# Optimization experiments

Hardware: AMD Instinct MI355X
Metric: run time of the kernel (lower is better)

## Reference

```python
import jax, jax.numpy as jnp
import numpy as np

P = 16          # patch_size
C = 3           # in_chans
D = 768         # embed_dim
V = 10240       # position_embedding_size
B, H, W = 16, 512, 512
N = (H // P) * (W // P)  # 1024 patches per image


def setup_inputs() -> dict:
    key = jax.random.key(0)
    k1, k2, k3, k4, k5 = jax.random.split(key, 5)
    pixel_values = jax.random.uniform(k1, (B, C, H, W), dtype=jnp.float32)
    position_ids = jax.random.randint(k2, (B, N, 2), 0, 32)  # (x, y) patch coords < pW/pH
    padding_positions = jax.random.randint(k3, (B, N), 0, 2).astype(jnp.bool_)
    w_proj = jax.random.normal(k4, (D, C * P * P), dtype=jnp.float32) * 0.02  # Linear weight (out, in)
    pos_table = jax.random.normal(k5, (2, V, D), dtype=jnp.float32) * 0.02
    return {
        "pixel_values": pixel_values,
        "w_proj": w_proj,
        "pos_table": pos_table,
        "position_ids": position_ids,
        "padding_positions": padding_positions,
    }


def reference(pixel_values, w_proj, pos_table, position_ids, padding_positions):
    b, c, h, w = pixel_values.shape
    ph, pw = h // P, w // P
    # Extract patches in Gemma4 C-P-P flatten order: (B, N, C*P*P)
    x = pixel_values.reshape(b, c, ph, P, pw, P)
    x = jnp.transpose(x, (0, 2, 4, 1, 3, 5)).reshape(b, ph * pw, c * P * P)
    patches = 2.0 * (x - 0.5)
    hidden = jnp.einsum('bnf,df->bnd', patches, w_proj)
    # Position embeddings: one_hot(ids) @ table summed over the 2 axes
    # == direct gather-add: table[0][x_id] + table[1][y_id]
    ids = jnp.clip(position_ids, 0)
    pos = pos_table[0][ids[..., 0]] + pos_table[1][ids[..., 1]]  # (B, N, D)
    pos = jnp.where(padding_positions[..., None], 0.0, pos)
    return hidden + pos
```

## Files before the change

kernel.cpp:

```cpp
#include <hip/hip_runtime.h>
#include <stdint.h>


typedef __attribute__((ext_vector_type(8))) short bfrag_t;
typedef __attribute__((ext_vector_type(4))) float f4_t;
typedef __attribute__((ext_vector_type(4))) unsigned short u16x4;

#define V_POS 10240
#define RS 40
#define ABUF 5120

__device__ __forceinline__ unsigned short f2bf(float f) {
    unsigned int u = __float_as_uint(f);
    u += 0x7fffu + ((u >> 16) & 1u);
    return (unsigned short)(u >> 16);
}

__device__ __forceinline__ void lgkm_barrier() {
    __builtin_amdgcn_s_waitcnt(0xC07F);
    __builtin_amdgcn_s_barrier();
}

__global__ __launch_bounds__(256, 2) void fused_kernel(
    const float* __restrict__ px, const float* __restrict__ wp,
    const int* __restrict__ pos_ids, const unsigned int* __restrict__ pad_in,
    const float* __restrict__ pos_table, float* __restrict__ out)
{
    __shared__ unsigned short LDS[4 * ABUF];

    const int tid  = threadIdx.x;
    const int wave = tid >> 6;
    const int lane = tid & 63;

    const int id   = blockIdx.x;
    const int xcd  = id & 7;
    const int slot = id >> 3;
    const int bmg  = slot / 6;
    const int bm   = xcd * 16 + bmg;
    const int bn   = slot - bmg * 6;
    const int m0   = bm << 7;
    const int n0   = bn << 7;
    const int bimg = bm >> 3;
    const int ph0  = (bm & 7) << 2;

    const bool u8mode = __any(pad_in[lane] > 1u);

    int aw[4], bw[4], bgb[4];
#pragma unroll
    for (int j = 0; j < 4; ++j) {
        int f4A = j * 64 + lane;
        int kh  = f4A >> 7;
        int f4i = f4A & 127;
        int pw  = f4i >> 2;
        int e   = f4i & 3;
        aw[j] = (wave * 32 + pw) * RS + kh * 16 + e * 4;
        int offb = j * 1024 + lane * 16;
        int colL = offb >> 7;
        int win  = offb & 127;
        bgb[j] = colL * 3072 + win;
        bw[j]  = (wave * 32 + colL) * RS + (win >> 2);
    }
    const float* abase = px + (((size_t)bimg * 3) * 512 + (size_t)(ph0 + wave) * 16) * 512;
    const char*  bbase = (const char*)(wp + (size_t)(n0 + wave * 32) * 768);
    const int    aglo  = lane * 4;

    float4 FA[2][4], FB[2][4];

    auto load_tile = [&](int t) {
        int s = t & 1;
        const float* ab = abase + (t >> 3) * 262144 + ((t * 2) & 15) * 512;
#pragma unroll
        for (int j = 0; j < 4; ++j)
            FA[s][j] = *(const float4*)(ab + j * 256 + aglo);
        const char* bb = bbase + t * 128;
#pragma unroll
        for (int j = 0; j < 4; ++j)
            FB[s][j] = *(const float4*)(bb + bgb[j]);
    };
    auto store_tile = [&](int t) {
        int s = t & 1;
        unsigned short* A = LDS + s * ABUF;
        unsigned short* B = LDS + 2 * ABUF + s * ABUF;
#pragma unroll
        for (int j = 0; j < 4; ++j) {
            u16x4 v;
            v[0] = f2bf(2.f * FA[s][j].x - 1.f);
            v[1] = f2bf(2.f * FA[s][j].y - 1.f);
            v[2] = f2bf(2.f * FA[s][j].z - 1.f);
            v[3] = f2bf(2.f * FA[s][j].w - 1.f);
            *(u16x4*)(A + aw[j]) = v;
            u16x4 w;
            w[0] = f2bf(FB[s][j].x);
            w[1] = f2bf(FB[s][j].y);
            w[2] = f2bf(FB[s][j].z);
            w[3] = f2bf(FB[s][j].w);
            *(u16x4*)(B + bw[j]) = w;
        }
    };

    const int fr      = lane & 15;
    const int quad    = lane >> 4;
    const int row_off = (wave & 1) << 6;
    const int col_off = (wave >> 1) << 6;

    f4_t acc[4][4] = {};

    load_tile(0);
    load_tile(1);
    store_tile(0);
    lgkm_barrier();

#pragma unroll
    for (int kk = 0; kk < 24; ++kk) {
        if (kk < 22) load_tile(kk + 2);
        if (kk < 23) store_tile(kk + 1);
        const unsigned short* Ab = LDS + (kk & 1) * ABUF + (row_off + fr) * RS + quad * 8;
        const unsigned short* Bb = LDS + 2 * ABUF + (kk & 1) * ABUF + (col_off + fr) * RS + quad * 8;
        bfrag_t a[4], b[4];
#pragma unroll
        for (int i = 0; i < 4; ++i) a[i] = *(const bfrag_t*)(Ab + i * 16 * RS);
#pragma unroll
        for (int i = 0; i < 4; ++i) b[i] = *(const bfrag_t*)(Bb + i * 16 * RS);
#pragma unroll
        for (int mi = 0; mi < 4; ++mi)
#pragma unroll
            for (int ni = 0; ni < 4; ++ni)
                acc[mi][ni] = __builtin_amdgcn_mfma_f32_16x16x32_bf16(
                    a[mi], b[ni], acc[mi][ni], 0, 0, 0);
        if (kk < 23) lgkm_barrier();
    }

    const unsigned char* pad8 = (const unsigned char*)pad_in;
    const int colbase = n0 + col_off;
#pragma unroll
    for (int mi = 0; mi < 4; ++mi) {
#pragma unroll
        for (int reg = 0; reg < 4; ++reg) {
            int gm  = m0 + row_off + mi * 16 + (quad << 2) + reg;
            int xid = pos_ids[2 * gm];
            int yid = pos_ids[2 * gm + 1];
            xid = xid < 0 ? 0 : xid;
            yid = yid < 0 ? 0 : yid;
            bool p = u8mode ? (pad8[gm] != 0) : (pad_in[gm] != 0u);
            const float* t0 = pos_table + (size_t)xid * 768 + colbase;
            const float* t1 = pos_table + (size_t)(V_POS + yid) * 768 + colbase;
            float* orow = out + (size_t)gm * 768 + colbase;
#pragma unroll
            for (int ni = 0; ni < 4; ++ni) {
                int cc = ni * 16 + fr;
                float pos = p ? 0.f : (t0[cc] + t1[cc]);
                orow[cc] = acc[mi][ni][reg] + pos;
            }
        }
    }
}

extern "C" void kernel_launch(void* const* d_in, const int* in_sizes, int n_in,
                              void* d_out, int out_size, void* d_ws, size_t ws_size,
                              hipStream_t stream) {
    const float*        px  = (const float*)d_in[0];
    const float*        wp  = (const float*)d_in[1];
    const float*        pt  = (const float*)d_in[2];
    const int*          pid = (const int*)d_in[3];
    const unsigned int* pad = (const unsigned int*)d_in[4];

    fused_kernel<<<768, 256, 0, stream>>>(px, wp, pid, pad, pt, (float*)d_out);
}
```

Before: 177.3 us.

## Split into bf16 prep kernel and async-LDS triple-buffered GEMM

Moves the patch extraction, normalization and bf16 conversion of pixels and weights into a separate prep kernel that writes a bf16 patch matrix and weight matrix to the workspace. The GEMM kernel then streams the bf16 tiles directly into LDS with global_load_lds, using a triple-buffered, XOR-swizzled layout and fewer barriers. The goal is to take the conversion work and register staging out of the main loop and overlap the loads better. In exchange it adds an extra launch and a round trip of the bf16 intermediates through global memory.

```diff
diff --git a/kernel.cpp b/kernel.cpp
--- a/kernel.cpp
+++ b/kernel.cpp
@@ -4,11 +4,10 @@
 
 typedef __attribute__((ext_vector_type(8))) short bfrag_t;
 typedef __attribute__((ext_vector_type(4))) float f4_t;
+typedef __attribute__((ext_vector_type(8))) unsigned short u16x8;
 typedef __attribute__((ext_vector_type(4))) unsigned short u16x4;
 
 #define V_POS 10240
-#define RS 40
-#define ABUF 5120
 
 __device__ __forceinline__ unsigned short f2bf(float f) {
     unsigned int u = __float_as_uint(f);
@@ -16,17 +15,62 @@
     return (unsigned short)(u >> 16);
 }
 
-__device__ __forceinline__ void lgkm_barrier() {
-    __builtin_amdgcn_s_waitcnt(0xC07F);
-    __builtin_amdgcn_s_barrier();
+__device__ __forceinline__ void async_ld16(const void* g, void* l) {
+    __builtin_amdgcn_global_load_lds(
+        (const __attribute__((address_space(1))) void*)g,
+        (__attribute__((address_space(3))) void*)l, 16, 0, 0);
 }
 
-__global__ __launch_bounds__(256, 2) void fused_kernel(
+__global__ __launch_bounds__(256) void prep_kernel(
     const float* __restrict__ px, const float* __restrict__ wp,
+    unsigned short* __restrict__ A, unsigned short* __restrict__ Wb)
+{
+    __shared__ unsigned short T[32 * 776];
+    int bid = blockIdx.x, tid = threadIdx.x;
+    if (bid < 512) {
+        int b = bid >> 5, ph = bid & 31;
+        const float* pxb = px + ((size_t)b * 3 * 512 + (size_t)ph * 16) * 512;
+#pragma unroll 6
+        for (int it = 0; it < 24; ++it) {
+            int idx = it * 256 + tid;
+            int c = idx >> 11, rem = idx & 2047, hl = rem >> 7, w4 = rem & 127;
+            float4 v = *(const float4*)(pxb + (size_t)c * 262144 + hl * 512 + (w4 << 2));
+            int pw  = w4 >> 2;
+            int pxo = (w4 & 3) << 2;
+            int k   = c * 256 + hl * 16 + pxo;
+            u16x4 o;
+            o[0] = f2bf(2.f * v.x - 1.f);
+            o[1] = f2bf(2.f * v.y - 1.f);
+            o[2] = f2bf(2.f * v.z - 1.f);
+            o[3] = f2bf(2.f * v.w - 1.f);
+            *(u16x4*)&T[pw * 776 + k] = o;
+        }
+        __syncthreads();
+        int r = tid >> 3, p = tid & 7;
+        unsigned short* Arow = A + ((size_t)bid * 32 + r) * 768;
+        const unsigned short* Trow = T + r * 776;
+#pragma unroll 4
+        for (int j = 0; j < 12; ++j) {
+            int co = (p + 8 * j) << 3;
+            *(u16x8*)(Arow + co) = *(const u16x8*)(Trow + co);
+        }
+    } else {
+        long idx = (long)(bid - 512) * 256 + tid;
+        const float4* s = (const float4*)(wp + (idx << 3));
+        float4 v0 = s[0], v1 = s[1];
+        u16x8 o;
+        o[0] = f2bf(v0.x); o[1] = f2bf(v0.y); o[2] = f2bf(v0.z); o[3] = f2bf(v0.w);
+        o[4] = f2bf(v1.x); o[5] = f2bf(v1.y); o[6] = f2bf(v1.z); o[7] = f2bf(v1.w);
+        *(u16x8*)(Wb + (idx << 3)) = o;
+    }
+}
+
+__global__ __launch_bounds__(256, 3) void gemm_kernel(
+    const unsigned short* __restrict__ A, const unsigned short* __restrict__ Bt,
     const int* __restrict__ pos_ids, const unsigned int* __restrict__ pad_in,
     const float* __restrict__ pos_table, float* __restrict__ out)
 {
-    __shared__ unsigned short LDS[4 * ABUF];
+    __shared__ unsigned short LDS[3 * 8192];
 
     const int tid  = threadIdx.x;
     const int wave = tid >> 6;
@@ -40,94 +84,65 @@
     const int bn   = slot - bmg * 6;
     const int m0   = bm << 7;
     const int n0   = bn << 7;
-    const int bimg = bm >> 3;
-    const int ph0  = (bm & 7) << 2;
 
     const bool u8mode = __any(pad_in[lane] > 1u);
 
-    int aw[4], bw[4], bgb[4];
-#pragma unroll
-    for (int j = 0; j < 4; ++j) {
-        int f4A = j * 64 + lane;
-        int kh  = f4A >> 7;
-        int f4i = f4A & 127;
-        int pw  = f4i >> 2;
-        int e   = f4i & 3;
-        aw[j] = (wave * 32 + pw) * RS + kh * 16 + e * 4;
-        int offb = j * 1024 + lane * 16;
-        int colL = offb >> 7;
-        int win  = offb & 127;
-        bgb[j] = colL * 3072 + win;
-        bw[j]  = (wave * 32 + colL) * RS + (win >> 2);
-    }
-    const float* abase = px + (((size_t)bimg * 3) * 512 + (size_t)(ph0 + wave) * 16) * 512;
-    const char*  bbase = (const char*)(wp + (size_t)(n0 + wave * 32) * 768);
-    const int    aglo  = lane * 4;
-
-    float4 FA[2][4], FB[2][4];
-
-    auto load_tile = [&](int t) {
-        int s = t & 1;
-        const float* ab = abase + (t >> 3) * 262144 + ((t * 2) & 15) * 512;
-#pragma unroll
-        for (int j = 0; j < 4; ++j)
-            FA[s][j] = *(const float4*)(ab + j * 256 + aglo);
-        const char* bb = bbase + t * 128;
-#pragma unroll
-        for (int j = 0; j < 4; ++j)
-            FB[s][j] = *(const float4*)(bb + bgb[j]);
-    };
-    auto store_tile = [&](int t) {
-        int s = t & 1;
-        unsigned short* A = LDS + s * ABUF;
-        unsigned short* B = LDS + 2 * ABUF + s * ABUF;
-#pragma unroll
-        for (int j = 0; j < 4; ++j) {
-            u16x4 v;
-            v[0] = f2bf(2.f * FA[s][j].x - 1.f);
-            v[1] = f2bf(2.f * FA[s][j].y - 1.f);
-            v[2] = f2bf(2.f * FA[s][j].z - 1.f);
-            v[3] = f2bf(2.f * FA[s][j].w - 1.f);
-            *(u16x4*)(A + aw[j]) = v;
-            u16x4 w;
-            w[0] = f2bf(FB[s][j].x);
-            w[1] = f2bf(FB[s][j].y);
-            w[2] = f2bf(FB[s][j].z);
-            w[3] = f2bf(FB[s][j].w);
-            *(u16x4*)(B + bw[j]) = w;
-        }
-    };
+    const int rl = lane >> 2;
+    const int g  = (lane & 3) ^ (rl & 3);
+    const unsigned short* aga0 = A  + (size_t)(m0 + wave * 32 + rl) * 768 + g * 8;
+    const unsigned short* aga1 = aga0 + (size_t)16 * 768;
+    const unsigned short* bga0 = Bt + (size_t)(n0 + wave * 32 + rl) * 768 + g * 8;
+    const unsigned short* bga1 = bga0 + (size_t)16 * 768;
+    const int l0 = wave * 32 * 32;
+    const int l1 = l0 + 16 * 32;
 
     const int fr      = lane & 15;
     const int quad    = lane >> 4;
     const int row_off = (wave & 1) << 6;
     const int col_off = (wave >> 1) << 6;
+    const int afro = (row_off + fr) * 32 + ((quad ^ (fr & 3)) << 3);
+    const int bfro = (col_off + fr) * 32 + ((quad ^ (fr & 3)) << 3) + 4096;
 
     f4_t acc[4][4] = {};
 
-    load_tile(0);
-    load_tile(1);
-    store_tile(0);
-    lgkm_barrier();
+    auto issue = [&](int t, int b) {
+        unsigned short* Ab = (unsigned short*)LDS + b * 8192;
+        unsigned short* Bb = Ab + 4096;
+        const int ko = t * 32;
+        async_ld16(aga0 + ko, Ab + l0);
+        async_ld16(aga1 + ko, Ab + l1);
+        async_ld16(bga0 + ko, Bb + l0);
+        async_ld16(bga1 + ko, Bb + l1);
+    };
 
-#pragma unroll
-    for (int kk = 0; kk < 24; ++kk) {
-        if (kk < 22) load_tile(kk + 2);
-        if (kk < 23) store_tile(kk + 1);
-        const unsigned short* Ab = LDS + (kk & 1) * ABUF + (row_off + fr) * RS + quad * 8;
-        const unsigned short* Bb = LDS + 2 * ABUF + (kk & 1) * ABUF + (col_off + fr) * RS + quad * 8;
+    issue(0, 0);
+    issue(1, 1);
+
+    int bi = 0;
+    for (int t = 0; t < 24; ++t) {
+        if (t < 23) __builtin_amdgcn_s_waitcnt(0xF74);
+        else        __builtin_amdgcn_s_waitcnt(0xF70);
+        __builtin_amdgcn_sched_barrier(0);
+        __builtin_amdgcn_s_barrier();
+        __builtin_amdgcn_sched_barrier(0);
+        if (t < 22) {
+            int nb = bi + 2; if (nb >= 3) nb -= 3;
+            issue(t + 2, nb);
+        }
+        const unsigned short* Ar = LDS + bi * 8192 + afro;
+        const unsigned short* Br = LDS + bi * 8192 + bfro;
         bfrag_t a[4], b[4];
 #pragma unroll
-        for (int i = 0; i < 4; ++i) a[i] = *(const bfrag_t*)(Ab + i * 16 * RS);
+        for (int i = 0; i < 4; ++i) a[i] = *(const bfrag_t*)(Ar + i * 512);
 #pragma unroll
-        for (int i = 0; i < 4; ++i) b[i] = *(const bfrag_t*)(Bb + i * 16 * RS);
+        for (int i = 0; i < 4; ++i) b[i] = *(const bfrag_t*)(Br + i * 512);
 #pragma unroll
         for (int mi = 0; mi < 4; ++mi)
 #pragma unroll
             for (int ni = 0; ni < 4; ++ni)
                 acc[mi][ni] = __builtin_amdgcn_mfma_f32_16x16x32_bf16(
                     a[mi], b[ni], acc[mi][ni], 0, 0, 0);
-        if (kk < 23) lgkm_barrier();
+        if (++bi == 3) bi = 0;
     }
 
     const unsigned char* pad8 = (const unsigned char*)pad_in;
@@ -164,5 +179,9 @@
     const int*          pid = (const int*)d_in[3];
     const unsigned int* pad = (const unsigned int*)d_in[4];
 
-    fused_kernel<<<768, 256, 0, stream>>>(px, wp, pid, pad, pt, (float*)d_out);
+    unsigned short* A  = (unsigned short*)d_ws;
+    unsigned short* Wb = A + (size_t)16384 * 768;
+
+    prep_kernel<<<800, 256, 0, stream>>>(px, wp, A, Wb);
+    gemm_kernel<<<768, 256, 0, stream>>>(A, Wb, pid, pad, pt, (float*)d_out);
 }
```

After: 179.2 us. About the same (+1.1%).
